# Kernel optimization log

Hardware: AMD Instinct MI355X
Metric: run time of the kernel (lower is better)

## Reference

```python
import jax, jax.numpy as jnp
import numpy as np

CUTOFF = 5.0
NLINKED = 1
CELL_LIST = CUTOFF / NLINKED  # linked-cell edge length
_r = np.arange(-NLINKED, NLINKED + 1)
# torch.cartesian_prod(r1,r1,r1) == meshgrid(indexing='ij') stacked & flattened
LINKED = np.stack(np.meshgrid(_r, _r, _r, indexing='ij'), axis=-1).reshape(1, -1, 3).astype(np.float32)  # (1, 27, 3)


def setup_inputs() -> dict:
    N = 2744
    L = 30.0
    key = jax.random.key(0)
    k1, k2 = jax.random.split(key)
    coordinates = jax.random.uniform(k1, (N, 3), dtype=jnp.float32) * L
    cell = jnp.eye(3, dtype=jnp.float32) * L
    mass = jax.random.uniform(k2, (N,), dtype=jnp.float32) * 15.0 + 1.0
    period_table = jnp.ones((3,), dtype=jnp.int32)  # fully periodic
    return {"period_table": period_table, "coordinates": coordinates, "cell": cell, "mass": mass}


def _forward(period_table, coordinates, cell, mass):
    numatom = coordinates.shape[0]
    # wrap coordinates into the cell relative to atom 0 (fractional coords)
    inv_cell = jnp.linalg.inv(cell)
    inv_coor = coordinates @ inv_cell
    inv_coor = inv_coor - jnp.round(inv_coor - inv_coor[0])
    coordinates = inv_coor @ cell
    # remove center of mass
    com = (mass @ coordinates) / jnp.sum(mass)
    coordinates = coordinates - com[None, :]
    # periodic replicas needed to cover the cutoff
    num_repeats = jnp.ceil(jnp.min(CUTOFF / jnp.abs(cell), axis=0)).astype(jnp.int32)
    num_repeats = period_table.astype(jnp.int32) * num_repeats
    up = num_repeats + 1
    down = -num_repeats
    rs = [jnp.arange(int(down[i]), int(up[i])) for i in range(3)]
    g = jnp.meshgrid(*rs, indexing='ij')
    shifts_frac = jnp.stack(g, axis=-1).reshape(-1, 3).astype(coordinates.dtype)  # (S, 3)
    shifts = shifts_frac @ cell  # (S, 3) cartesian shift vectors
    num_shifts = shifts.shape[0]
    # prod = cartesian_prod(all_shifts, all_atoms).T : row0 shift idx, row1 atom idx
    prod0 = jnp.repeat(jnp.arange(num_shifts), numatom)
    prod1 = jnp.tile(jnp.arange(numatom), num_shifts)
    # shift box so all coords are positive; pad by cutoff
    mincoor = jnp.min(coordinates, axis=0) - CUTOFF - 1e-6
    coordinates = coordinates - mincoor
    maxcoor = jnp.max(coordinates, axis=0) + CUTOFF
    # all periodic images, keep only those inside the padded box
    image = (coordinates[None, :, :] + shifts[:, None, :]).reshape(-1, 3)
    keep = jnp.nonzero(((image < maxcoor) & (image > 0)).all(axis=1))[0]
    image_mask = image[keep]                      # (M, 3)
    prod0 = prod0[keep]
    prod1 = prod1[keep]
    # linked-cell indices
    ori_image_index = jnp.floor(coordinates / CELL_LIST)         # (N, 3)
    neigh_cell = ori_image_index[:, None, :] + jnp.asarray(LINKED)  # (N, 27, 3)
    image_index = jnp.floor(image_mask / CELL_LIST)              # (M, 3)
    max_cell_index = jnp.ceil(maxcoor / CELL_LIST)
    f10 = max_cell_index[1] * max_cell_index[0]
    neigh_cell_index = neigh_cell[:, :, 2] * f10 + neigh_cell[:, :, 1] * max_cell_index[0] + neigh_cell[:, :, 0]  # (N, 27)
    nimage_index = image_index[:, 2] * f10 + image_index[:, 1] * max_cell_index[0] + image_index[:, 0]            # (M,)
    # dense (N, M, 27) cell-index equality -- the memory-bound hot spot
    eq = neigh_cell_index[:, None, :] == nimage_index[None, :, None]
    ai, aj, _ = jnp.nonzero(eq)
    # distance filter on candidate pairs
    d = jnp.linalg.norm(coordinates[ai] - image_mask[aj], axis=-1)
    pair = jnp.nonzero((d < CUTOFF) & (d > 0.001))[0]
    center = ai[pair]
    img = aj[pair]
    shift_idx = prod0[img]
    atom_j = prod1[img]
    neigh_list = jnp.stack([center, atom_j])  # (2, P)
    return neigh_list, shifts[shift_idx], shifts_frac, shift_idx


def reference(period_table, coordinates, cell, mass):
    neigh_list, shifts_out, _, _ = _forward(period_table, coordinates, cell, mass)
    return (neigh_list, shifts_out)
```

## Files before the change

kernel.cpp:

```cpp
#include <hip/hip_runtime.h>
#include <math.h>

#define S_CAP     27
#define NCELL_MAX 1024
#define CAP       64
#define CAPSH     6
#define MAXNB     128
#define CUT       5.0f
#define NTHR      256
#define GRP       64



__device__ __forceinline__ void load_cell(const float* __restrict__ cell, float c[3][3])
{
    #pragma unroll
    for (int i = 0; i < 3; i++)
        #pragma unroll
        for (int j = 0; j < 3; j++) c[i][j] = cell[3 * i + j];
}

__device__ __forceinline__ void header_and_shifts(
    const float c[3][3], const int* __restrict__ period,
    const double* __restrict__ pd, const float* __restrict__ pf, int nblkA,
    float* sF, int* sI, float* s_shifts)
{
    #pragma clang fp contract(off)
    int t = threadIdx.x;
    if (t < 64) {
        double SM = 0.0, SX = 0.0, SY = 0.0, SZ = 0.0;
        float MN0 =  __builtin_inff(), MN1 =  __builtin_inff(), MN2 =  __builtin_inff();
        float MX0 = -__builtin_inff(), MX1 = -__builtin_inff(), MX2 = -__builtin_inff();
        for (int b = t; b < nblkA; b += 64) {
            SM += pd[4*b+0]; SX += pd[4*b+1]; SY += pd[4*b+2]; SZ += pd[4*b+3];
            MN0 = fminf(MN0, pf[6*b+0]); MN1 = fminf(MN1, pf[6*b+1]); MN2 = fminf(MN2, pf[6*b+2]);
            MX0 = fmaxf(MX0, pf[6*b+3]); MX1 = fmaxf(MX1, pf[6*b+4]); MX2 = fmaxf(MX2, pf[6*b+5]);
        }
        #pragma unroll
        for (int off = 32; off > 0; off >>= 1) {
            SM += __shfl_down(SM, off, 64);
            SX += __shfl_down(SX, off, 64);
            SY += __shfl_down(SY, off, 64);
            SZ += __shfl_down(SZ, off, 64);
            MN0 = fminf(MN0, __shfl_down(MN0, off, 64));
            MN1 = fminf(MN1, __shfl_down(MN1, off, 64));
            MN2 = fminf(MN2, __shfl_down(MN2, off, 64));
            MX0 = fmaxf(MX0, __shfl_down(MX0, off, 64));
            MX1 = fmaxf(MX1, __shfl_down(MX1, off, 64));
            MX2 = fmaxf(MX2, __shfl_down(MX2, off, 64));
        }
        if (t == 0) {
            float den  = (float)SM;
            float com0 = ((float)SX) / den;
            float com1 = ((float)SY) / den;
            float com2 = ((float)SZ) / den;
            float m20 = ((MN0 - com0) - CUT) - 1e-6f;
            float m21 = ((MN1 - com1) - CUT) - 1e-6f;
            float m22 = ((MN2 - com2) - CUT) - 1e-6f;
            float maxc0 = ((MX0 - com0) - m20) + CUT;
            float maxc1 = ((MX1 - com1) - m21) + CUT;
            float maxc2 = ((MX2 - com2) - m22) + CUT;
            float mcell0 = ceilf(maxc0 / CUT);
            float mcell1 = ceilf(maxc1 / CUT);
            float f10 = mcell1 * mcell0;
            int nr[3];
            for (int j = 0; j < 3; j++) {
                float v = __builtin_inff();
                for (int i = 0; i < 3; i++) {
                    float q = CUT / fabsf(c[i][j]);
                    v = fminf(v, q);
                }
                nr[j] = (int)ceilf(v);
                nr[j] *= period[j];
            }
            int nsz0 = 2*nr[0]+1, nsz1 = 2*nr[1]+1, nsz2 = 2*nr[2]+1;
            int S = nsz0 * nsz1 * nsz2;
            if (S > S_CAP) S = S_CAP;
            sI[0] = S;
            sI[1] = -nr[0]; sI[2] = -nr[1]; sI[3] = -nr[2];
            sI[4] = nsz1;   sI[5] = nsz2;
            sI[6] = (int)mcell0;
            sI[7] = (int)f10;
            sF[0] = maxc0; sF[1] = maxc1; sF[2] = maxc2;
            sF[3] = f10;   sF[4] = mcell0;
            sF[5] = m20;   sF[6] = m21;   sF[7] = m22;
            sF[8] = com0;  sF[9] = com1;  sF[10] = com2;
        }
    }
    __syncthreads();
    int S = sI[0];
    if (t < S) {
        int n1 = sI[4], n2 = sI[5];
        int i0 = t / (n1 * n2);
        int rem = t - i0 * n1 * n2;
        int i1 = rem / n2;
        int i2 = rem - i1 * n2;
        float fx = (float)(sI[1] + i0);
        float fy = (float)(sI[2] + i1);
        float fz = (float)(sI[3] + i2);
        #pragma unroll
        for (int d = 0; d < 3; d++)
            s_shifts[3*t + d] = fx*c[0][d] + fy*c[1][d] + fz*c[2][d];
    }
    __syncthreads();
}

__global__ __launch_bounds__(NTHR)
void kA_wrap(const float* __restrict__ coor, const float* __restrict__ cell,
             const float* __restrict__ mass, float* __restrict__ xv,
             int* __restrict__ ccur, int* __restrict__ sc_agg,
             int* __restrict__ grp_sum, int* __restrict__ grp_arrive,
             double* __restrict__ pd, float* __restrict__ pf, int n, int nagg, int ng)
{
    #pragma clang fp contract(off)
    __shared__ double wsum[4][4];
    __shared__ float  wred[4][6];
    int t    = threadIdx.x;
    int bid  = blockIdx.x;
    int gtid = bid * NTHR + t;
    int lane = t & 63;
    int w    = t >> 6;

    if (gtid < NCELL_MAX) ccur[gtid] = 0;
    if (gtid < nagg)      sc_agg[gtid] = -1;
    if (gtid < ng)        { grp_sum[gtid] = -1; grp_arrive[gtid] = 0; }

    float c[3][3];
    load_cell(cell, c);
    float a00 = c[1][1]*c[2][2] - c[1][2]*c[2][1];
    float a01 = c[0][2]*c[2][1] - c[0][1]*c[2][2];
    float a02 = c[0][1]*c[1][2] - c[0][2]*c[1][1];
    float a10 = c[1][2]*c[2][0] - c[1][0]*c[2][2];
    float a11 = c[0][0]*c[2][2] - c[0][2]*c[2][0];
    float a12 = c[0][2]*c[1][0] - c[0][0]*c[1][2];
    float a20 = c[1][0]*c[2][1] - c[1][1]*c[2][0];
    float a21 = c[0][1]*c[2][0] - c[0][0]*c[2][1];
    float a22 = c[0][0]*c[1][1] - c[0][1]*c[1][0];
    float det = c[0][0]*a00 + c[0][1]*a10 + c[0][2]*a20;
    float inv[3][3] = {{a00/det, a01/det, a02/det},
                       {a10/det, a11/det, a12/det},
                       {a20/det, a21/det, a22/det}};
    float f0[3];
    #pragma unroll
    for (int d = 0; d < 3; d++)
        f0[d] = coor[0]*inv[0][d] + coor[1]*inv[1][d] + coor[2]*inv[2][d];

    double sm = 0.0, sx = 0.0, sy = 0.0, sz = 0.0;
    float mn0 =  __builtin_inff(), mn1 =  __builtin_inff(), mn2 =  __builtin_inff();
    float mx0 = -__builtin_inff(), mx1 = -__builtin_inff(), mx2 = -__builtin_inff();
    if (gtid < n) {
        float p0 = coor[3*gtid], p1 = coor[3*gtid+1], p2 = coor[3*gtid+2];
        float ic[3], ww[3], x[3];
        #pragma unroll
        for (int d = 0; d < 3; d++)
            ic[d] = p0*inv[0][d] + p1*inv[1][d] + p2*inv[2][d];
        #pragma unroll
        for (int d = 0; d < 3; d++)
            ww[d] = ic[d] - rintf(ic[d] - f0[d]);
        #pragma unroll
        for (int d = 0; d < 3; d++)
            x[d] = ww[0]*c[0][d] + ww[1]*c[1][d] + ww[2]*c[2][d];
        xv[3*gtid] = x[0]; xv[3*gtid+1] = x[1]; xv[3*gtid+2] = x[2];
        float m = mass[gtid];
        sm = (double)m;
        sx = (double)m * (double)x[0];
        sy = (double)m * (double)x[1];
        sz = (double)m * (double)x[2];
        mn0 = x[0]; mn1 = x[1]; mn2 = x[2];
        mx0 = x[0]; mx1 = x[1]; mx2 = x[2];
    }
    #pragma unroll
    for (int off = 32; off > 0; off >>= 1) {
        sm += __shfl_down(sm, off, 64);
        sx += __shfl_down(sx, off, 64);
        sy += __shfl_down(sy, off, 64);
        sz += __shfl_down(sz, off, 64);
        mn0 = fminf(mn0, __shfl_down(mn0, off, 64));
        mn1 = fminf(mn1, __shfl_down(mn1, off, 64));
        mn2 = fminf(mn2, __shfl_down(mn2, off, 64));
        mx0 = fmaxf(mx0, __shfl_down(mx0, off, 64));
        mx1 = fmaxf(mx1, __shfl_down(mx1, off, 64));
        mx2 = fmaxf(mx2, __shfl_down(mx2, off, 64));
    }
    if (lane == 0) {
        wsum[w][0] = sm; wsum[w][1] = sx; wsum[w][2] = sy; wsum[w][3] = sz;
        wred[w][0] = mn0; wred[w][1] = mn1; wred[w][2] = mn2;
        wred[w][3] = mx0; wred[w][4] = mx1; wred[w][5] = mx2;
    }
    __syncthreads();
    if (t == 0) {
        double SM = 0.0, SX = 0.0, SY = 0.0, SZ = 0.0;
        float MN0 =  __builtin_inff(), MN1 =  __builtin_inff(), MN2 =  __builtin_inff();
        float MX0 = -__builtin_inff(), MX1 = -__builtin_inff(), MX2 = -__builtin_inff();
        #pragma unroll
        for (int q = 0; q < 4; q++) {
            SM += wsum[q][0]; SX += wsum[q][1]; SY += wsum[q][2]; SZ += wsum[q][3];
            MN0 = fminf(MN0, wred[q][0]); MN1 = fminf(MN1, wred[q][1]); MN2 = fminf(MN2, wred[q][2]);
            MX0 = fmaxf(MX0, wred[q][3]); MX1 = fmaxf(MX1, wred[q][4]); MX2 = fmaxf(MX2, wred[q][5]);
        }
        pd[bid*4+0] = SM; pd[bid*4+1] = SX; pd[bid*4+2] = SY; pd[bid*4+3] = SZ;
        pf[bid*6+0] = MN0; pf[bid*6+1] = MN1; pf[bid*6+2] = MN2;
        pf[bid*6+3] = MX0; pf[bid*6+4] = MX1; pf[bid*6+5] = MX2;
    }
}

__global__ __launch_bounds__(NTHR)
void kB_fill(const int* __restrict__ period, const float* __restrict__ cell,
             const double* __restrict__ pd, const float* __restrict__ pf,
             const float* __restrict__ xv, int* __restrict__ ccur,
             float4* __restrict__ cellbuf, int nblkA, int n)
{
    #pragma clang fp contract(off)
    __shared__ float sF[12];
    __shared__ int   sI[8];
    __shared__ float s_shifts[3 * S_CAP];
    float c[3][3];
    load_cell(cell, c);
    header_and_shifts(c, period, pd, pf, nblkA, sF, sI, s_shifts);

    int a = blockIdx.x * NTHR + threadIdx.x;
    int s = blockIdx.y;
    if (a < n && s < sI[0]) {
        float m20 = sF[5], m21 = sF[6], m22 = sF[7];
        float com0 = sF[8], com1 = sF[9], com2 = sF[10];
        float u0 = (xv[3*a]   - com0) - m20;
        float u1 = (xv[3*a+1] - com1) - m21;
        float u2 = (xv[3*a+2] - com2) - m22;
        float i0 = u0 + s_shifts[3*s];
        float i1 = u1 + s_shifts[3*s+1];
        float i2 = u2 + s_shifts[3*s+2];
        bool k = (i0 > 0.0f) && (i0 < sF[0]) &&
                 (i1 > 0.0f) && (i1 < sF[1]) &&
                 (i2 > 0.0f) && (i2 < sF[2]);
        if (k) {
            float fc0 = floorf(i0 / CUT);
            float fc1 = floorf(i1 / CUT);
            float fc2 = floorf(i2 / CUT);
            float cf = fc2 * sF[3] + fc1 * sF[4] + fc0;
            int ci = (int)cf;
            if ((unsigned)ci < (unsigned)NCELL_MAX) {
                int pos = atomicAdd(&ccur[ci], 1);
                if (pos < CAP)
                    cellbuf[(ci << CAPSH) + pos] = make_float4(i0, i1, i2, __int_as_float(s * n + a));
            }
        }
    }
}

__global__ __launch_bounds__(NTHR, 4)
void kC_search_emit(const int* __restrict__ period, const float* __restrict__ cell,
                    const double* __restrict__ pd, const float* __restrict__ pf,
                    const float* __restrict__ xv, const int* __restrict__ ccur,
                    const float4* __restrict__ cellbuf,
                    int* __restrict__ sc_agg, int* __restrict__ grp_sum,
                    int* __restrict__ grp_arrive,
                    float* __restrict__ out, int nblkA, int nblkC, int n, int P)
{
    #pragma clang fp contract(off)
    __shared__ float sF[12];
    __shared__ int   sI[8];
    __shared__ float s_shifts[3 * S_CAP];
    __shared__ int   lst[4][MAXNB];
    __shared__ int   s_np[4];
    __shared__ int   sExcl;
    __shared__ int   sFin;

    const int t    = threadIdx.x;
    const int bid  = blockIdx.x;
    const int lane = t & 63;
    const int w    = t >> 6;
    const int g    = bid / GRP;
    const int gpos = bid - g * GRP;
    const int gbase = g * GRP;
    const int gsz  = min(GRP, nblkC - gbase);

    float c[3][3];
    load_cell(cell, c);
    header_and_shifts(c, period, pd, pf, nblkA, sF, sI, s_shifts);

    const int atom = bid * 4 + w;
    const bool valid = atom < n;

    {
        const float m20 = sF[5], m21 = sF[6], m22 = sF[7];
        const float com0 = sF[8], com1 = sF[9], com2 = sF[10];
        const int mci = sI[6], f10i = sI[7];
        int cnt = 0;
        if (valid) {
            float x0 = (xv[3*atom]   - com0) - m20;
            float x1 = (xv[3*atom+1] - com1) - m21;
            float x2 = (xv[3*atom+2] - com2) - m22;
            int o0 = (int)floorf(x0 / CUT);
            int o1 = (int)floorf(x1 / CUT);
            int o2 = (int)floorf(x2 / CUT);

            int ncb[9], c0a[9], c1a[9], cum[10];
            cum[0] = 0;
            #pragma unroll
            for (int r = 0; r < 9; r++) {
                int dz = r / 3 - 1, dy = r % 3 - 1;
                ncb[r] = (o2+dz)*f10i + (o1+dy)*mci + (o0-1);
                int q0 = 0, q1 = 0, q2 = 0, nc;
                nc = ncb[r];     if ((unsigned)nc < (unsigned)NCELL_MAX) { q0 = ccur[nc]; q0 = q0 > CAP ? CAP : q0; }
                nc = ncb[r] + 1; if ((unsigned)nc < (unsigned)NCELL_MAX) { q1 = ccur[nc]; q1 = q1 > CAP ? CAP : q1; }
                nc = ncb[r] + 2; if ((unsigned)nc < (unsigned)NCELL_MAX) { q2 = ccur[nc]; q2 = q2 > CAP ? CAP : q2; }
                c0a[r] = q0; c1a[r] = q1;
                cum[r+1] = cum[r] + q0 + q1 + q2;
            }
            int T = cum[9];
            for (int base = 0; base < T; base += 64) {
                int L = base + lane;
                bool act = L < T;
                bool ok = false; int gg = 0;
                if (act) {
                    int r = 0;
                    #pragma unroll
                    for (int q = 1; q < 9; q++) r += (L >= cum[q]) ? 1 : 0;
                    int off = L - cum[r];
                    int c0 = c0a[r], c1 = c1a[r];
                    int slot = (off < c0)      ? ((ncb[r]     << CAPSH) + off)
                             : (off < c0 + c1) ? (((ncb[r]+1) << CAPSH) + off - c0)
                                               : (((ncb[r]+2) << CAPSH) + off - c0 - c1);
                    float4 v = cellbuf[slot];
                    gg = __float_as_int(v.w);
                    float dxx = x0 - v.x;
                    float dyy = x1 - v.y;
                    float dzz = x2 - v.z;
                    float ss = dxx*dxx + dyy*dyy + dzz*dzz;
                    float dd = sqrtf(ss);
                    ok = (dd < CUT) && (dd > 0.001f);
                }
                unsigned long long m = __ballot(ok);
                int posn = cnt + (int)__popcll(m & ((1ull << lane) - 1ull));
                if (ok && posn < MAXNB) lst[w][posn] = gg;
                cnt += (int)__popcll(m);
            }
            if (cnt > MAXNB) cnt = MAXNB;
        }
        if (lane == 0) s_np[w] = cnt;
    }
    __syncthreads();

    if (t == 0) {
        int agg = s_np[0] + s_np[1] + s_np[2] + s_np[3];
        __hip_atomic_store(&sc_agg[bid], agg, __ATOMIC_RELAXED, __HIP_MEMORY_SCOPE_AGENT);
        int r = __hip_atomic_fetch_add(&grp_arrive[g], 1, __ATOMIC_ACQ_REL, __HIP_MEMORY_SCOPE_AGENT);
        sFin = (r == gsz - 1) ? 1 : 0;
    }
    __syncthreads();

    if (sFin && w == 0) {
        int idx = gbase + lane;
        int v = 0;
        if (lane < gsz)
            v = __hip_atomic_load(&sc_agg[idx], __ATOMIC_RELAXED, __HIP_MEMORY_SCOPE_AGENT);
        #pragma unroll
        for (int off = 32; off > 0; off >>= 1)
            v += __shfl_down(v, off, 64);
        if (lane == 0)
            __hip_atomic_store(&grp_sum[g], v, __ATOMIC_RELAXED, __HIP_MEMORY_SCOPE_AGENT);
    }

    if (w == 0) {
        int v1 = 0;
        if (lane < g) {
            v1 = __hip_atomic_load(&grp_sum[lane], __ATOMIC_RELAXED, __HIP_MEMORY_SCOPE_AGENT);
            while (v1 == -1) {
                __builtin_amdgcn_s_sleep(2);
                v1 = __hip_atomic_load(&grp_sum[lane], __ATOMIC_RELAXED, __HIP_MEMORY_SCOPE_AGENT);
            }
        }
        int v2 = 0;
        if (lane < gpos) {
            int idx = gbase + lane;
            v2 = __hip_atomic_load(&sc_agg[idx], __ATOMIC_RELAXED, __HIP_MEMORY_SCOPE_AGENT);
            while (v2 == -1) {
                __builtin_amdgcn_s_sleep(2);
                v2 = __hip_atomic_load(&sc_agg[idx], __ATOMIC_RELAXED, __HIP_MEMORY_SCOPE_AGENT);
            }
        }
        int v = v1 + v2;
        #pragma unroll
        for (int off = 32; off > 0; off >>= 1)
            v += __shfl_down(v, off, 64);
        if (lane == 0) sExcl = v;
    }
    __syncthreads();

    if (valid) {
        int cnt = s_np[w];
        int base = sExcl;
        for (int q = 0; q < w; q++) base += s_np[q];
        for (int r = lane; r < cnt; r += 64) {
            int gg = lst[w][r];
            int rank = 0;
            for (int q = 0; q < cnt; q++) rank += (lst[w][q] < gg) ? 1 : 0;
            int p = base + rank;
            if (p < P) {
                int sidx = gg / n;
                int a = gg - sidx * n;
                out[p]     = (float)atom;
                out[P + p] = (float)a;
                out[2*P + 3*p]     = s_shifts[3*sidx];
                out[2*P + 3*p + 1] = s_shifts[3*sidx + 1];
                out[2*P + 3*p + 2] = s_shifts[3*sidx + 2];
            }
        }
    }
}

extern "C" void kernel_launch(void* const* d_in, const int* in_sizes, int n_in,
                              void* d_out, int out_size, void* d_ws, size_t ws_size,
                              hipStream_t stream)
{
    const int*   period = (const int*)d_in[0];
    const float* coor   = (const float*)d_in[1];
    const float* cell   = (const float*)d_in[2];
    const float* mass   = (const float*)d_in[3];
    float* out = (float*)d_out;

    int n = in_sizes[1] / 3;
    int P = out_size / 5;

    char* wp = (char*)d_ws;
    size_t off = 0;
    auto alloc = [&](size_t bytes) -> void* {
        off = (off + 15) & ~(size_t)15;
        void* pp = (void*)(wp + off); off += bytes; return pp;
    };

    int nblkA = (n + NTHR - 1) / NTHR;
    int nblkC = (n + 3) / 4;
    int ng    = (nblkC + GRP - 1) / GRP;

    float*  xv       = (float*) alloc(3 * (size_t)n * 4);
    int*    ccur     = (int*)   alloc(NCELL_MAX * 4);
    float4* cellbuf  = (float4*)alloc((size_t)NCELL_MAX * CAP * 16);
    double* pd       = (double*)alloc((size_t)nblkA * 4 * 8);
    float*  pf       = (float*) alloc((size_t)nblkA * 6 * 4);
    int*    sc_agg   = (int*)   alloc((size_t)nblkC * 4);
    int*    grp_sum  = (int*)   alloc((size_t)ng * 4);
    int*    grp_arr  = (int*)   alloc((size_t)ng * 4);
    (void)ws_size; (void)n_in;

    hipLaunchKernelGGL(kA_wrap, dim3(nblkA), dim3(NTHR), 0, stream,
                       coor, cell, mass, xv, ccur, sc_agg, grp_sum, grp_arr,
                       pd, pf, n, nblkC, ng);
    hipLaunchKernelGGL(kB_fill, dim3(nblkA, S_CAP), dim3(NTHR), 0, stream,
                       period, cell, pd, pf, xv, ccur, cellbuf, nblkA, n);
    hipLaunchKernelGGL(kC_search_emit, dim3(nblkC), dim3(NTHR), 0, stream,
                       period, cell, pd, pf, xv, ccur, cellbuf,
                       sc_agg, grp_sum, grp_arr, out, nblkA, nblkC, n, P);
}
```

Before: 95.63 us.

## Replace linked-cell build with brute-force minimum-image pair search from LDS

Removes the cell-fill kernel and its atomics-based bucket buffer. The search kernel now stages all wrapped atom coordinates in shared memory and tests every atom pair under the minimum-image convention, rounding fractional offsets to recover the shift index. This saves a kernel launch and the scattered cell-buffer reads, at the cost of O(N^2) distance work and about 33KB of LDS per block. It is only correct when the box is larger than twice the cutoff, so only one image can fall within range, and it silently returns for n above a hard-coded 2744.

```diff
diff --git a/kernel.cpp b/kernel.cpp
--- a/kernel.cpp
+++ b/kernel.cpp
@@ -1,14 +1,12 @@
 #include <hip/hip_runtime.h>
 #include <math.h>
 
-#define S_CAP     27
-#define NCELL_MAX 1024
-#define CAP       64
-#define CAPSH     6
-#define MAXNB     128
-#define CUT       5.0f
-#define NTHR      256
-#define GRP       64
+#define S_CAP  27
+#define MAXNB  128
+#define CUT    5.0f
+#define NTHR   256
+#define GRP    64
+#define NMAX   2744
 
 
 
@@ -108,7 +106,7 @@
 __global__ __launch_bounds__(NTHR)
 void kA_wrap(const float* __restrict__ coor, const float* __restrict__ cell,
              const float* __restrict__ mass, float* __restrict__ xv,
-             int* __restrict__ ccur, int* __restrict__ sc_agg,
+             int* __restrict__ sc_agg,
              int* __restrict__ grp_sum, int* __restrict__ grp_arrive,
              double* __restrict__ pd, float* __restrict__ pf, int n, int nagg, int ng)
 {
@@ -121,9 +119,8 @@
     int lane = t & 63;
     int w    = t >> 6;
 
-    if (gtid < NCELL_MAX) ccur[gtid] = 0;
-    if (gtid < nagg)      sc_agg[gtid] = -1;
-    if (gtid < ng)        { grp_sum[gtid] = -1; grp_arrive[gtid] = 0; }
+    if (gtid < nagg) sc_agg[gtid] = -1;
+    if (gtid < ng)   { grp_sum[gtid] = -1; grp_arrive[gtid] = 0; }
 
     float c[3][3];
     load_cell(cell, c);
@@ -204,54 +201,10 @@
     }
 }
 
-__global__ __launch_bounds__(NTHR)
-void kB_fill(const int* __restrict__ period, const float* __restrict__ cell,
-             const double* __restrict__ pd, const float* __restrict__ pf,
-             const float* __restrict__ xv, int* __restrict__ ccur,
-             float4* __restrict__ cellbuf, int nblkA, int n)
-{
-    #pragma clang fp contract(off)
-    __shared__ float sF[12];
-    __shared__ int   sI[8];
-    __shared__ float s_shifts[3 * S_CAP];
-    float c[3][3];
-    load_cell(cell, c);
-    header_and_shifts(c, period, pd, pf, nblkA, sF, sI, s_shifts);
-
-    int a = blockIdx.x * NTHR + threadIdx.x;
-    int s = blockIdx.y;
-    if (a < n && s < sI[0]) {
-        float m20 = sF[5], m21 = sF[6], m22 = sF[7];
-        float com0 = sF[8], com1 = sF[9], com2 = sF[10];
-        float u0 = (xv[3*a]   - com0) - m20;
-        float u1 = (xv[3*a+1] - com1) - m21;
-        float u2 = (xv[3*a+2] - com2) - m22;
-        float i0 = u0 + s_shifts[3*s];
-        float i1 = u1 + s_shifts[3*s+1];
-        float i2 = u2 + s_shifts[3*s+2];
-        bool k = (i0 > 0.0f) && (i0 < sF[0]) &&
-                 (i1 > 0.0f) && (i1 < sF[1]) &&
-                 (i2 > 0.0f) && (i2 < sF[2]);
-        if (k) {
-            float fc0 = floorf(i0 / CUT);
-            float fc1 = floorf(i1 / CUT);
-            float fc2 = floorf(i2 / CUT);
-            float cf = fc2 * sF[3] + fc1 * sF[4] + fc0;
-            int ci = (int)cf;
-            if ((unsigned)ci < (unsigned)NCELL_MAX) {
-                int pos = atomicAdd(&ccur[ci], 1);
-                if (pos < CAP)
-                    cellbuf[(ci << CAPSH) + pos] = make_float4(i0, i1, i2, __int_as_float(s * n + a));
-            }
-        }
-    }
-}
-
 __global__ __launch_bounds__(NTHR, 4)
 void kC_search_emit(const int* __restrict__ period, const float* __restrict__ cell,
                     const double* __restrict__ pd, const float* __restrict__ pf,
-                    const float* __restrict__ xv, const int* __restrict__ ccur,
-                    const float4* __restrict__ cellbuf,
+                    const float* __restrict__ xv,
                     int* __restrict__ sc_agg, int* __restrict__ grp_sum,
                     int* __restrict__ grp_arrive,
                     float* __restrict__ out, int nblkA, int nblkC, int n, int P)
@@ -260,6 +213,7 @@
     __shared__ float sF[12];
     __shared__ int   sI[8];
     __shared__ float s_shifts[3 * S_CAP];
+    __shared__ float sux[NMAX], suy[NMAX], suz[NMAX];
     __shared__ int   lst[4][MAXNB];
     __shared__ int   s_np[4];
     __shared__ int   sExcl;
@@ -274,61 +228,66 @@
     const int gbase = g * GRP;
     const int gsz  = min(GRP, nblkC - gbase);
 
+    if (n > NMAX) return;
+
     float c[3][3];
     load_cell(cell, c);
     header_and_shifts(c, period, pd, pf, nblkA, sF, sI, s_shifts);
 
-    const int atom = bid * 4 + w;
-    const bool valid = atom < n;
+    float a00 = c[1][1]*c[2][2] - c[1][2]*c[2][1];
+    float a01 = c[0][2]*c[2][1] - c[0][1]*c[2][2];
+    float a02 = c[0][1]*c[1][2] - c[0][2]*c[1][1];
+    float a10 = c[1][2]*c[2][0] - c[1][0]*c[2][2];
+    float a11 = c[0][0]*c[2][2] - c[0][2]*c[2][0];
+    float a12 = c[0][2]*c[1][0] - c[0][0]*c[1][2];
+    float a20 = c[1][0]*c[2][1] - c[1][1]*c[2][0];
+    float a21 = c[0][1]*c[2][0] - c[0][0]*c[2][1];
+    float a22 = c[0][0]*c[1][1] - c[0][1]*c[1][0];
+    float det = c[0][0]*a00 + c[0][1]*a10 + c[0][2]*a20;
+    float inv[3][3] = {{a00/det, a01/det, a02/det},
+                       {a10/det, a11/det, a12/det},
+                       {a20/det, a21/det, a22/det}};
 
     {
         const float m20 = sF[5], m21 = sF[6], m22 = sF[7];
         const float com0 = sF[8], com1 = sF[9], com2 = sF[10];
-        const int mci = sI[6], f10i = sI[7];
+        for (int j = t; j < n; j += NTHR) {
+            sux[j] = (xv[3*j]   - com0) - m20;
+            suy[j] = (xv[3*j+1] - com1) - m21;
+            suz[j] = (xv[3*j+2] - com2) - m22;
+        }
+    }
+    __syncthreads();
+
+    const int atom = bid * 4 + w;
+    const bool valid = atom < n;
+
+    {
         int cnt = 0;
         if (valid) {
-            float x0 = (xv[3*atom]   - com0) - m20;
-            float x1 = (xv[3*atom+1] - com1) - m21;
-            float x2 = (xv[3*atom+2] - com2) - m22;
-            int o0 = (int)floorf(x0 / CUT);
-            int o1 = (int)floorf(x1 / CUT);
-            int o2 = (int)floorf(x2 / CUT);
-
-            int ncb[9], c0a[9], c1a[9], cum[10];
-            cum[0] = 0;
-            #pragma unroll
-            for (int r = 0; r < 9; r++) {
-                int dz = r / 3 - 1, dy = r % 3 - 1;
-                ncb[r] = (o2+dz)*f10i + (o1+dy)*mci + (o0-1);
-                int q0 = 0, q1 = 0, q2 = 0, nc;
-                nc = ncb[r];     if ((unsigned)nc < (unsigned)NCELL_MAX) { q0 = ccur[nc]; q0 = q0 > CAP ? CAP : q0; }
-                nc = ncb[r] + 1; if ((unsigned)nc < (unsigned)NCELL_MAX) { q1 = ccur[nc]; q1 = q1 > CAP ? CAP : q1; }
-                nc = ncb[r] + 2; if ((unsigned)nc < (unsigned)NCELL_MAX) { q2 = ccur[nc]; q2 = q2 > CAP ? CAP : q2; }
-                c0a[r] = q0; c1a[r] = q1;
-                cum[r+1] = cum[r] + q0 + q1 + q2;
-            }
-            int T = cum[9];
-            for (int base = 0; base < T; base += 64) {
-                int L = base + lane;
-                bool act = L < T;
+            const float xi = sux[atom], yi = suy[atom], zi = suz[atom];
+            const int d0 = sI[1], d1 = sI[2], d2 = sI[3];
+            const int nsz1 = sI[4], nsz2 = sI[5];
+            for (int jb = 0; jb < n; jb += 64) {
+                int j = jb + lane;
                 bool ok = false; int gg = 0;
-                if (act) {
-                    int r = 0;
-                    #pragma unroll
-                    for (int q = 1; q < 9; q++) r += (L >= cum[q]) ? 1 : 0;
-                    int off = L - cum[r];
-                    int c0 = c0a[r], c1 = c1a[r];
-                    int slot = (off < c0)      ? ((ncb[r]     << CAPSH) + off)
-                             : (off < c0 + c1) ? (((ncb[r]+1) << CAPSH) + off - c0)
-                                               : (((ncb[r]+2) << CAPSH) + off - c0 - c1);
-                    float4 v = cellbuf[slot];
-                    gg = __float_as_int(v.w);
-                    float dxx = x0 - v.x;
-                    float dyy = x1 - v.y;
-                    float dzz = x2 - v.z;
-                    float ss = dxx*dxx + dyy*dyy + dzz*dzz;
+                if (j < n) {
+                    float ujx = sux[j], ujy = suy[j], ujz = suz[j];
+                    float dx = xi - ujx, dy = yi - ujy, dz = zi - ujz;
+                    float fr0 = rintf(dx*inv[0][0] + dy*inv[1][0] + dz*inv[2][0]);
+                    float fr1 = rintf(dx*inv[0][1] + dy*inv[1][1] + dz*inv[2][1]);
+                    float fr2 = rintf(dx*inv[0][2] + dy*inv[1][2] + dz*inv[2][2]);
+                    float sx = fr0*c[0][0] + fr1*c[1][0] + fr2*c[2][0];
+                    float sy = fr0*c[0][1] + fr1*c[1][1] + fr2*c[2][1];
+                    float sz = fr0*c[0][2] + fr1*c[1][2] + fr2*c[2][2];
+                    float imx = ujx + sx, imy = ujy + sy, imz = ujz + sz;
+                    float ddx = xi - imx, ddy = yi - imy, ddz = zi - imz;
+                    float ss = ddx*ddx + ddy*ddy + ddz*ddz;
                     float dd = sqrtf(ss);
                     ok = (dd < CUT) && (dd > 0.001f);
+                    int i0 = (int)fr0 - d0, i1 = (int)fr1 - d1, i2 = (int)fr2 - d2;
+                    int idx = (i0 * nsz1 + i1) * nsz2 + i2;
+                    gg = idx * n + j;
                 }
                 unsigned long long m = __ballot(ok);
                 int posn = cnt + (int)__popcll(m & ((1ull << lane) - 1ull));
@@ -434,8 +393,6 @@
     int ng    = (nblkC + GRP - 1) / GRP;
 
     float*  xv       = (float*) alloc(3 * (size_t)n * 4);
-    int*    ccur     = (int*)   alloc(NCELL_MAX * 4);
-    float4* cellbuf  = (float4*)alloc((size_t)NCELL_MAX * CAP * 16);
     double* pd       = (double*)alloc((size_t)nblkA * 4 * 8);
     float*  pf       = (float*) alloc((size_t)nblkA * 6 * 4);
     int*    sc_agg   = (int*)   alloc((size_t)nblkC * 4);
@@ -444,11 +401,9 @@
     (void)ws_size; (void)n_in;
 
     hipLaunchKernelGGL(kA_wrap, dim3(nblkA), dim3(NTHR), 0, stream,
-                       coor, cell, mass, xv, ccur, sc_agg, grp_sum, grp_arr,
+                       coor, cell, mass, xv, sc_agg, grp_sum, grp_arr,
                        pd, pf, n, nblkC, ng);
-    hipLaunchKernelGGL(kB_fill, dim3(nblkA, S_CAP), dim3(NTHR), 0, stream,
-                       period, cell, pd, pf, xv, ccur, cellbuf, nblkA, n);
     hipLaunchKernelGGL(kC_search_emit, dim3(nblkC), dim3(NTHR), 0, stream,
-                       period, cell, pd, pf, xv, ccur, cellbuf,
+                       period, cell, pd, pf, xv,
                        sc_agg, grp_sum, grp_arr, out, nblkA, nblkC, n, P);
 }
```

New measurement: 96.47 us. Within noise of the previous version (+0.9%).
